# Optimization experiments

Measured on AMD Instinct MI355X. Metric: run time of the kernel, lower is better.

## Reference

```python
import jax, jax.numpy as jnp
import numpy as np

B, S, D = 32, 1, 4096
H, HKV, HD = 32, 8, 128
G = H // HKV            # GQA groups = 4
MAXLEN = 2048
START = 2047            # decode position; cache holds 2047 past tokens


def setup_inputs() -> dict:
    key = jax.random.key(0)
    ks = jax.random.split(key, 8)
    w_scale = 0.02
    # RoPE angles for position START (module works only for seq_len==1)
    inv_freq = 1.0 / (10000.0 ** (np.arange(0, HD, 2, dtype=np.float32) / HD))
    ang = jnp.asarray(START * inv_freq, dtype=jnp.float32)  # (HD/2,)
    return {
        "x": jax.random.normal(ks[0], (B, S, D), jnp.float32),
        "cache_k": jax.random.normal(ks[1], (B, HKV, MAXLEN, HD), jnp.float32),
        "cache_v": jax.random.normal(ks[2], (B, HKV, MAXLEN, HD), jnp.float32),
        "wq": jax.random.normal(ks[3], (D, H * HD), jnp.float32) * w_scale,
        "wk": jax.random.normal(ks[4], (D, HKV * HD), jnp.float32) * w_scale,
        "wv": jax.random.normal(ks[5], (D, HKV * HD), jnp.float32) * w_scale,
        "wo": jax.random.normal(ks[6], (H * HD, D), jnp.float32) * w_scale,
        "freqs_cos": jnp.cos(ang),
        "freqs_sin": jnp.sin(ang),
        "start_pos": START,
    }


def _rope(x, cos, sin):
    # x: (B, h, S, HD); complex multiply on interleaved (even=real, odd=imag) pairs
    xr, xi = x[..., 0::2], x[..., 1::2]
    out_r = xr * cos - xi * sin
    out_i = xr * sin + xi * cos
    return jnp.stack([out_r, out_i], axis=-1).reshape(x.shape)


def reference(x, cache_k, cache_v, wq, wk, wv, wo, freqs_cos, freqs_sin, start_pos):
    b, s, _ = x.shape
    # projections -> (B, heads, S, HD)
    q = (x @ wq).reshape(b, s, H, HD).transpose(0, 2, 1, 3)
    k = (x @ wk).reshape(b, s, HKV, HD).transpose(0, 2, 1, 3)
    v = (x @ wv).reshape(b, s, HKV, HD).transpose(0, 2, 1, 3)
    # RoPE on q and k
    q = _rope(q, freqs_cos, freqs_sin)
    k = _rope(k, freqs_cos, freqs_sin)
    # KV-cache append at start_pos
    ck = jax.lax.dynamic_update_slice(cache_k, k, (0, 0, start_pos, 0))
    cv = jax.lax.dynamic_update_slice(cache_v, v, (0, 0, start_pos, 0))
    L = start_pos + s
    keys = ck[:, :, :L]   # (B, HKV, L, HD)
    vals = cv[:, :, :L]
    # GQA: group query heads over kv heads (avoids materializing repeat_kv;
    # identical math to expand+reshape in the original)
    qg = q.reshape(b, HKV, G, s, HD)
    scale = 1.0 / np.sqrt(HD).astype(np.float32)
    scores = jnp.einsum('bkgsd,bkld->bkgsl', qg, keys) * scale
    probs = jax.nn.softmax(scores.astype(jnp.float32), axis=-1).astype(q.dtype)
    out = jnp.einsum('bkgsl,bkld->bkgsd', probs, vals)
    out = out.reshape(b, H, s, HD).transpose(0, 2, 1, 3).reshape(b, s, H * HD)
    return out @ wo
```

## Files before the change

kernel.cpp:

```cpp
#include <hip/hip_runtime.h>
#include <cmath>

#define Bb 32
#define Dm 4096
#define Hh 32
#define HKVh 8
#define HD 128
#define Gq 4
#define MAXLEN 2048
#define NQ 4096
#define NKV 1024
#define NTOT 6144
#define KSPLIT 8
#define KCH 512
#define LSPLIT 4
#define SCALE 0.08838834764831845f

__device__ __forceinline__ float4 fma4(float s, float4 w, float4 a) {
    a.x = fmaf(s, w.x, a.x); a.y = fmaf(s, w.y, a.y);
    a.z = fmaf(s, w.z, a.z); a.w = fmaf(s, w.w, a.w);
    return a;
}

__global__ __launch_bounds__(256) void k_qkv(const float* __restrict__ x,
    const float* __restrict__ wq, const float* __restrict__ wk,
    const float* __restrict__ wv, float* __restrict__ part)
{
    __shared__ float xs[Bb][KCH];
    const int ct = blockIdx.x;
    const int ks = blockIdx.y;
    const int c0 = ct * 64;
    const int k0 = ks * KCH;
    const float* Wp; int ldw; int cw;
    if (c0 < NQ)          { Wp = wq; ldw = NQ;  cw = c0; }
    else if (c0 < NQ+NKV) { Wp = wk; ldw = NKV; cw = c0 - NQ; }
    else                  { Wp = wv; ldw = NKV; cw = c0 - NQ - NKV; }

    const int t = threadIdx.x;
    for (int i = t; i < Bb * (KCH/4); i += 256) {
        int b = i >> 7;
        int kk = (i & 127) << 2;
        float4 v4 = *(const float4*)(x + (size_t)b*Dm + k0 + kk);
        xs[b][kk+0] = v4.x; xs[b][kk+1] = v4.y; xs[b][kk+2] = v4.z; xs[b][kk+3] = v4.w;
    }
    __syncthreads();

    const int cg = t & 15;
    const int bg = t >> 4;
    const int b0 = bg * 2;
    const float* wp = Wp + (size_t)k0 * ldw + cw + cg*4;
    float4 a0 = make_float4(0.f,0.f,0.f,0.f), a1 = make_float4(0.f,0.f,0.f,0.f);
#pragma unroll 2
    for (int k = 0; k < KCH; k += 4) {
        float4 w0 = *(const float4*)(wp);
        float4 w1 = *(const float4*)(wp + ldw);
        float4 w2 = *(const float4*)(wp + 2*ldw);
        float4 w3 = *(const float4*)(wp + 3*ldw);
        wp += 4*ldw;
        float4 xa = *(const float4*)(&xs[b0][k]);
        float4 xb = *(const float4*)(&xs[b0+1][k]);
        a0 = fma4(xa.x, w0, a0); a1 = fma4(xb.x, w0, a1);
        a0 = fma4(xa.y, w1, a0); a1 = fma4(xb.y, w1, a1);
        a0 = fma4(xa.z, w2, a0); a1 = fma4(xb.z, w2, a1);
        a0 = fma4(xa.w, w3, a0); a1 = fma4(xb.w, w3, a1);
    }
    size_t base = ((size_t)ks * Bb + b0) * NTOT + c0 + cg*4;
    *(float4*)(part + base) = a0;
    *(float4*)(part + base + NTOT) = a1;
}

__global__ __launch_bounds__(256) void k_rope_scatter(const float* __restrict__ part,
    const float* __restrict__ cos_, const float* __restrict__ sin_,
    const int* __restrict__ start_pos, float* __restrict__ qbuf,
    float* __restrict__ cache_k, float* __restrict__ cache_v)
{
    int idx = blockIdx.x*256 + threadIdx.x;
    int b  = idx / (NTOT/2);
    int cp = idx % (NTOT/2);
    int c = cp*2;
    float xr = 0.f, xi = 0.f;
#pragma unroll
    for (int s = 0; s < KSPLIT; ++s) {
        const float2 p = *(const float2*)(part + ((size_t)s*Bb + b)*NTOT + c);
        xr += p.x; xi += p.y;
    }
    const int sp = start_pos[0];
    if (c < NQ) {
        int h = c / HD, dd = c % HD; int fi = dd >> 1;
        float co = cos_[fi], si = sin_[fi];
        float2 o = make_float2(xr*co - xi*si, xr*si + xi*co);
        *(float2*)(qbuf + ((size_t)b*Hh + h)*HD + dd) = o;
    } else if (c < NQ+NKV) {
        int cc = c - NQ; int h = cc / HD, dd = cc % HD; int fi = dd >> 1;
        float co = cos_[fi], si = sin_[fi];
        float2 o = make_float2(xr*co - xi*si, xr*si + xi*co);
        *(float2*)(cache_k + (((size_t)b*HKVh + h)*MAXLEN + sp)*HD + dd) = o;
    } else {
        int cc = c - NQ - NKV; int h = cc / HD, dd = cc % HD;
        *(float2*)(cache_v + (((size_t)b*HKVh + h)*MAXLEN + sp)*HD + dd) = make_float2(xr, xi);
    }
}

__global__ __launch_bounds__(512) void k_attn(const float* __restrict__ qbuf,
    const float* __restrict__ cache_k, const float* __restrict__ cache_v,
    const int* __restrict__ start_pos, float* __restrict__ pout)
{
    __shared__ float sbuf[Gq][128];
    __shared__ float mrun[Gq], lrun[Gq], alphaS[Gq];
    __shared__ float pbuf[4][Gq][HD];

    const int bk = blockIdx.x;
    const int b  = bk >> 3;
    const int kv = bk & 7;
    const int sp = blockIdx.y;
    const int L  = start_pos[0] + 1;
    const int per = (L + LSPLIT - 1) / LSPLIT;
    const int p0 = sp * per;
    const int p1 = min(L, p0 + per);

    const int t = threadIdx.x;
    const int wave = t >> 6;
    const int lane = t & 63;
    const int half = lane >> 5;
    const int dl = lane & 31;

    float4 q4[Gq];
#pragma unroll
    for (int g = 0; g < Gq; ++g)
        q4[g] = *(const float4*)(qbuf + ((size_t)b*Hh + kv*Gq + g)*HD + dl*4);

    const float* kbase = cache_k + ((size_t)b*HKVh + kv)*MAXLEN*HD;
    const float* vbase = cache_v + ((size_t)b*HKVh + kv)*MAXLEN*HD;

    const int dC = t & 127;
    const int psC = t >> 7;
    float acc[Gq] = {0.f,0.f,0.f,0.f};

    if (t < Gq) { mrun[t] = -INFINITY; lrun[t] = 0.f; }
    __syncthreads();

    for (int c0 = p0; c0 < p1; c0 += 128) {
        const int CP = min(128, p1 - c0);
        for (int j = wave; j < 64; j += 8) {
            int p = c0 + 2*j + half;
            int pc = p < p1 ? p : (p1 - 1);
            float4 k4 = *(const float4*)(kbase + (size_t)pc*HD + dl*4);
            float s0 = q4[0].x*k4.x + q4[0].y*k4.y + q4[0].z*k4.z + q4[0].w*k4.w;
            float s1 = q4[1].x*k4.x + q4[1].y*k4.y + q4[1].z*k4.z + q4[1].w*k4.w;
            float s2 = q4[2].x*k4.x + q4[2].y*k4.y + q4[2].z*k4.z + q4[2].w*k4.w;
            float s3 = q4[3].x*k4.x + q4[3].y*k4.y + q4[3].z*k4.z + q4[3].w*k4.w;
#pragma unroll
            for (int off = 16; off; off >>= 1) {
                s0 += __shfl_xor(s0, off, 32);
                s1 += __shfl_xor(s1, off, 32);
                s2 += __shfl_xor(s2, off, 32);
                s3 += __shfl_xor(s3, off, 32);
            }
            if (dl == 0) {
                int slot = 2*j + half;
                bool ok = (p < p1);
                sbuf[0][slot] = ok ? s0*SCALE : -INFINITY;
                sbuf[1][slot] = ok ? s1*SCALE : -INFINITY;
                sbuf[2][slot] = ok ? s2*SCALE : -INFINITY;
                sbuf[3][slot] = ok ? s3*SCALE : -INFINITY;
            }
        }
        __syncthreads();
        if (wave < Gq) {
            int g = wave;
            float s0 = sbuf[g][lane];
            float s1 = sbuf[g][lane + 64];
            float mloc = fmaxf(s0, s1);
#pragma unroll
            for (int off = 32; off; off >>= 1) mloc = fmaxf(mloc, __shfl_xor(mloc, off));
            float mold = mrun[g];
            float mnew = fmaxf(mold, mloc);
            float e0 = __expf(s0 - mnew);
            float e1 = __expf(s1 - mnew);
            sbuf[g][lane]      = e0;
            sbuf[g][lane + 64] = e1;
            float ssum = e0 + e1;
#pragma unroll
            for (int off = 32; off; off >>= 1) ssum += __shfl_xor(ssum, off);
            if (lane == 0) {
                float alpha = (mold == -INFINITY) ? 0.f : __expf(mold - mnew);
                alphaS[g] = alpha;
                lrun[g] = lrun[g]*alpha + ssum;
                mrun[g] = mnew;
            }
        }
        __syncthreads();
        {
#pragma unroll
            for (int g = 0; g < Gq; ++g) acc[g] *= alphaS[g];
            for (int p = c0 + psC; p < c0 + CP; p += 4) {
                float vv = vbase[(size_t)p*HD + dC];
#pragma unroll
                for (int g = 0; g < Gq; ++g)
                    acc[g] = fmaf(sbuf[g][p - c0], vv, acc[g]);
            }
        }
        __syncthreads();
    }
#pragma unroll
    for (int g = 0; g < Gq; ++g) pbuf[psC][g][dC] = acc[g];
    __syncthreads();
    float* po = pout + (size_t)(bk * LSPLIT + sp) * (Gq*HD + 2*Gq);
    {
        int g = t >> 7, d = t & 127;
        float s = pbuf[0][g][d] + pbuf[1][g][d] + pbuf[2][g][d] + pbuf[3][g][d];
        po[g*HD + d] = s;
    }
    if (t < Gq) { po[Gq*HD + t] = mrun[t]; po[Gq*HD + Gq + t] = lrun[t]; }
}

__global__ __launch_bounds__(256) void k_comb(const float* __restrict__ pout,
    float* __restrict__ attn)
{
    int idx = blockIdx.x*256 + threadIdx.x;
    int d = idx & 127;
    int h = (idx >> 7) & 31;
    int b = idx >> 12;
    int kv = h >> 2, g = h & 3;
    int bk = b*8 + kv;
    const float* base = pout + (size_t)bk * LSPLIT * (Gq*HD + 2*Gq);
    float m = -INFINITY;
#pragma unroll
    for (int s = 0; s < LSPLIT; ++s) m = fmaxf(m, base[s*520 + 512 + g]);
    float num = 0.f, den = 0.f;
#pragma unroll
    for (int s = 0; s < LSPLIT; ++s) {
        float ms = base[s*520 + 512 + g];
        float ls = base[s*520 + 516 + g];
        float w = (ms == -INFINITY) ? 0.f : __expf(ms - m);
        num = fmaf(w, base[s*520 + g*HD + d], num);
        den = fmaf(w, ls, den);
    }
    attn[idx] = num / den;
}

__global__ __launch_bounds__(256) void k_proj(const float* __restrict__ inp,
    const float* __restrict__ W, float* __restrict__ part)
{
    __shared__ float xs[Bb][KCH];
    const int ct = blockIdx.x;
    const int ks = blockIdx.y;
    const int c0 = ct * 64;
    const int k0 = ks * KCH;

    const int t = threadIdx.x;
    for (int i = t; i < Bb * (KCH/4); i += 256) {
        int b = i >> 7;
        int kk = (i & 127) << 2;
        float4 v4 = *(const float4*)(inp + (size_t)b*NQ + k0 + kk);
        xs[b][kk+0] = v4.x; xs[b][kk+1] = v4.y; xs[b][kk+2] = v4.z; xs[b][kk+3] = v4.w;
    }
    __syncthreads();

    const int cg = t & 15;
    const int bg = t >> 4;
    const int b0 = bg * 2;
    const float* wp = W + (size_t)k0 * NQ + c0 + cg*4;
    float4 a0 = make_float4(0.f,0.f,0.f,0.f), a1 = make_float4(0.f,0.f,0.f,0.f);
#pragma unroll 2
    for (int k = 0; k < KCH; k += 4) {
        float4 w0 = *(const float4*)(wp);
        float4 w1 = *(const float4*)(wp + NQ);
        float4 w2 = *(const float4*)(wp + 2*NQ);
        float4 w3 = *(const float4*)(wp + 3*NQ);
        wp += 4*NQ;
        float4 xa = *(const float4*)(&xs[b0][k]);
        float4 xb = *(const float4*)(&xs[b0+1][k]);
        a0 = fma4(xa.x, w0, a0); a1 = fma4(xb.x, w0, a1);
        a0 = fma4(xa.y, w1, a0); a1 = fma4(xb.y, w1, a1);
        a0 = fma4(xa.z, w2, a0); a1 = fma4(xb.z, w2, a1);
        a0 = fma4(xa.w, w3, a0); a1 = fma4(xb.w, w3, a1);
    }
    size_t base = ((size_t)ks * Bb + b0) * NQ + c0 + cg*4;
    *(float4*)(part + base) = a0;
    *(float4*)(part + base + NQ) = a1;
}

__global__ __launch_bounds__(256) void k_red(const float* __restrict__ part,
    float* __restrict__ out)
{
    int idx = blockIdx.x*256 + threadIdx.x;
    float s = 0.f;
#pragma unroll
    for (int k = 0; k < KSPLIT; ++k) s += part[(size_t)k*Bb*NQ + idx];
    out[idx] = s;
}

extern "C" void kernel_launch(void* const* d_in, const int* in_sizes, int n_in,
                              void* d_out, int out_size, void* d_ws, size_t ws_size,
                              hipStream_t stream)
{
    const float* x  = (const float*)d_in[0];
    float* cache_k  = (float*)d_in[1];
    float* cache_v  = (float*)d_in[2];
    const float* wq = (const float*)d_in[3];
    const float* wk = (const float*)d_in[4];
    const float* wv = (const float*)d_in[5];
    const float* wo = (const float*)d_in[6];
    const float* fc = (const float*)d_in[7];
    const float* fs = (const float*)d_in[8];
    const int* sp   = (const int*)d_in[9];
    float* out      = (float*)d_out;

    float* ws = (float*)d_ws;
    float* qkv_part = ws;
    float* qbuf     = qkv_part + 1572864;
    float* attn_prt = qbuf + 131072;
    float* attn_out = attn_prt + 532480;
    float* proj_prt = attn_out + 131072;

    k_qkv<<<dim3(96, 8), 256, 0, stream>>>(x, wq, wk, wv, qkv_part);
    k_rope_scatter<<<dim3(384), 256, 0, stream>>>(qkv_part, fc, fs, sp, qbuf, cache_k, cache_v);
    k_attn<<<dim3(256, LSPLIT), 512, 0, stream>>>(qbuf, cache_k, cache_v, sp, attn_prt);
    k_comb<<<dim3(512), 256, 0, stream>>>(attn_prt, attn_out);
    k_proj<<<dim3(64, 8), 256, 0, stream>>>(attn_out, wo, proj_prt);
    k_red<<<dim3(512), 256, 0, stream>>>(proj_prt, out);
}
```

Measured before the change: 751.6 us.

## Restructure decode attention into per-wave online softmax without block barriers

Each of the 8 waves in the attention block now owns a contiguous slice of the sequence range. Within that slice it streams K and V together, keeps the running max, sum and output accumulator in registers, and folds the softmax scale into q. This replaces the earlier per-128-position chunk loop, which staged scores in shared memory behind three block-wide barriers and used a separate pass for the softmax and the V accumulation. Partial results are merged once, first across the two half-waves and then across waves through shared memory. The aim is to remove barrier stalls and overlap K and V memory traffic. The cost is more exp calls per position and higher register pressure from float4 accumulators for four groups.

```diff
diff --git a/kernel.cpp b/kernel.cpp
--- a/kernel.cpp
+++ b/kernel.cpp
@@ -105,9 +105,9 @@
     const float* __restrict__ cache_k, const float* __restrict__ cache_v,
     const int* __restrict__ start_pos, float* __restrict__ pout)
 {
-    __shared__ float sbuf[Gq][128];
-    __shared__ float mrun[Gq], lrun[Gq], alphaS[Gq];
-    __shared__ float pbuf[4][Gq][HD];
+    __shared__ float sm[8][Gq];
+    __shared__ float sl[8][Gq];
+    __shared__ float sacc[8][Gq][HD];
 
     const int bk = blockIdx.x;
     const int b  = bk >> 3;
@@ -122,96 +122,130 @@
     const int wave = t >> 6;
     const int lane = t & 63;
     const int half = lane >> 5;
-    const int dl = lane & 31;
+    const int dl   = lane & 31;
 
     float4 q4[Gq];
 #pragma unroll
-    for (int g = 0; g < Gq; ++g)
-        q4[g] = *(const float4*)(qbuf + ((size_t)b*Hh + kv*Gq + g)*HD + dl*4);
+    for (int g = 0; g < Gq; ++g) {
+        float4 qq = *(const float4*)(qbuf + ((size_t)b*Hh + kv*Gq + g)*HD + dl*4);
+        qq.x *= SCALE; qq.y *= SCALE; qq.z *= SCALE; qq.w *= SCALE;
+        q4[g] = qq;
+    }
 
     const float* kbase = cache_k + ((size_t)b*HKVh + kv)*MAXLEN*HD;
     const float* vbase = cache_v + ((size_t)b*HKVh + kv)*MAXLEN*HD;
 
-    const int dC = t & 127;
-    const int psC = t >> 7;
-    float acc[Gq] = {0.f,0.f,0.f,0.f};
-
-    if (t < Gq) { mrun[t] = -INFINITY; lrun[t] = 0.f; }
+    const int nw  = (per + 7) >> 3;
+    const int wp0 = p0 + wave * nw;
+    const int wp1 = min(p1, wp0 + nw);
+
+    float  m[Gq], l[Gq];
+    float4 acc[Gq];
+#pragma unroll
+    for (int g = 0; g < Gq; ++g) {
+        m[g] = -1e30f; l[g] = 0.f;
+        acc[g] = make_float4(0.f, 0.f, 0.f, 0.f);
+    }
+
+    for (int pp = wp0; pp < wp1; pp += 4) {
+        const int pa = pp + half;
+        const int pb = pp + 2 + half;
+        const bool va = pa < wp1;
+        const bool vb = pb < wp1;
+        const int pca = va ? pa : wp0;
+        const int pcb = vb ? pb : wp0;
+        const float4 kA = *(const float4*)(kbase + (size_t)pca*HD + dl*4);
+        const float4 kB = *(const float4*)(kbase + (size_t)pcb*HD + dl*4);
+        const float4 vA = *(const float4*)(vbase + (size_t)pca*HD + dl*4);
+        const float4 vB = *(const float4*)(vbase + (size_t)pcb*HD + dl*4);
+
+        float sA[Gq], sB[Gq];
+#pragma unroll
+        for (int g = 0; g < Gq; ++g) {
+            sA[g] = q4[g].x*kA.x + q4[g].y*kA.y + q4[g].z*kA.z + q4[g].w*kA.w;
+            sB[g] = q4[g].x*kB.x + q4[g].y*kB.y + q4[g].z*kB.z + q4[g].w*kB.w;
+        }
+#pragma unroll
+        for (int off = 16; off; off >>= 1) {
+#pragma unroll
+            for (int g = 0; g < Gq; ++g) {
+                sA[g] += __shfl_xor(sA[g], off);
+                sB[g] += __shfl_xor(sB[g], off);
+            }
+        }
+        if (!va) { sA[0] = -INFINITY; sA[1] = -INFINITY; sA[2] = -INFINITY; sA[3] = -INFINITY; }
+        if (!vb) { sB[0] = -INFINITY; sB[1] = -INFINITY; sB[2] = -INFINITY; sB[3] = -INFINITY; }
+
+#pragma unroll
+        for (int g = 0; g < Gq; ++g) {
+            float mn = fmaxf(m[g], sA[g]);
+            float al = __expf(m[g] - mn);
+            float e  = __expf(sA[g] - mn);
+            m[g] = mn;
+            l[g] = l[g]*al + e;
+            acc[g].x = fmaf(e, vA.x, acc[g].x*al);
+            acc[g].y = fmaf(e, vA.y, acc[g].y*al);
+            acc[g].z = fmaf(e, vA.z, acc[g].z*al);
+            acc[g].w = fmaf(e, vA.w, acc[g].w*al);
+        }
+#pragma unroll
+        for (int g = 0; g < Gq; ++g) {
+            float mn = fmaxf(m[g], sB[g]);
+            float al = __expf(m[g] - mn);
+            float e  = __expf(sB[g] - mn);
+            m[g] = mn;
+            l[g] = l[g]*al + e;
+            acc[g].x = fmaf(e, vB.x, acc[g].x*al);
+            acc[g].y = fmaf(e, vB.y, acc[g].y*al);
+            acc[g].z = fmaf(e, vB.z, acc[g].z*al);
+            acc[g].w = fmaf(e, vB.w, acc[g].w*al);
+        }
+    }
+
+#pragma unroll
+    for (int g = 0; g < Gq; ++g) {
+        float mo = __shfl_xor(m[g], 32);
+        float lo = __shfl_xor(l[g], 32);
+        float ax = __shfl_xor(acc[g].x, 32);
+        float ay = __shfl_xor(acc[g].y, 32);
+        float az = __shfl_xor(acc[g].z, 32);
+        float aw = __shfl_xor(acc[g].w, 32);
+        float mn = fmaxf(m[g], mo);
+        float a0 = __expf(m[g] - mn);
+        float a1 = __expf(mo - mn);
+        m[g] = mn;
+        l[g] = l[g]*a0 + lo*a1;
+        acc[g].x = acc[g].x*a0 + ax*a1;
+        acc[g].y = acc[g].y*a0 + ay*a1;
+        acc[g].z = acc[g].z*a0 + az*a1;
+        acc[g].w = acc[g].w*a0 + aw*a1;
+    }
+
+    if (half == 0) {
+#pragma unroll
+        for (int g = 0; g < Gq; ++g) {
+            *(float4*)(&sacc[wave][g][dl*4]) = acc[g];
+            if (dl == 0) { sm[wave][g] = m[g]; sl[wave][g] = l[g]; }
+        }
+    }
     __syncthreads();
 
-    for (int c0 = p0; c0 < p1; c0 += 128) {
-        const int CP = min(128, p1 - c0);
-        for (int j = wave; j < 64; j += 8) {
-            int p = c0 + 2*j + half;
-            int pc = p < p1 ? p : (p1 - 1);
-            float4 k4 = *(const float4*)(kbase + (size_t)pc*HD + dl*4);
-            float s0 = q4[0].x*k4.x + q4[0].y*k4.y + q4[0].z*k4.z + q4[0].w*k4.w;
-            float s1 = q4[1].x*k4.x + q4[1].y*k4.y + q4[1].z*k4.z + q4[1].w*k4.w;
-            float s2 = q4[2].x*k4.x + q4[2].y*k4.y + q4[2].z*k4.z + q4[2].w*k4.w;
-            float s3 = q4[3].x*k4.x + q4[3].y*k4.y + q4[3].z*k4.z + q4[3].w*k4.w;
-#pragma unroll
-            for (int off = 16; off; off >>= 1) {
-                s0 += __shfl_xor(s0, off, 32);
-                s1 += __shfl_xor(s1, off, 32);
-                s2 += __shfl_xor(s2, off, 32);
-                s3 += __shfl_xor(s3, off, 32);
-            }
-            if (dl == 0) {
-                int slot = 2*j + half;
-                bool ok = (p < p1);
-                sbuf[0][slot] = ok ? s0*SCALE : -INFINITY;
-                sbuf[1][slot] = ok ? s1*SCALE : -INFINITY;
-                sbuf[2][slot] = ok ? s2*SCALE : -INFINITY;
-                sbuf[3][slot] = ok ? s3*SCALE : -INFINITY;
-            }
-        }
-        __syncthreads();
-        if (wave < Gq) {
-            int g = wave;
-            float s0 = sbuf[g][lane];
-            float s1 = sbuf[g][lane + 64];
-            float mloc = fmaxf(s0, s1);
-#pragma unroll
-            for (int off = 32; off; off >>= 1) mloc = fmaxf(mloc, __shfl_xor(mloc, off));
-            float mold = mrun[g];
-            float mnew = fmaxf(mold, mloc);
-            float e0 = __expf(s0 - mnew);
-            float e1 = __expf(s1 - mnew);
-            sbuf[g][lane]      = e0;
-            sbuf[g][lane + 64] = e1;
-            float ssum = e0 + e1;
-#pragma unroll
-            for (int off = 32; off; off >>= 1) ssum += __shfl_xor(ssum, off);
-            if (lane == 0) {
-                float alpha = (mold == -INFINITY) ? 0.f : __expf(mold - mnew);
-                alphaS[g] = alpha;
-                lrun[g] = lrun[g]*alpha + ssum;
-                mrun[g] = mnew;
-            }
-        }
-        __syncthreads();
-        {
-#pragma unroll
-            for (int g = 0; g < Gq; ++g) acc[g] *= alphaS[g];
-            for (int p = c0 + psC; p < c0 + CP; p += 4) {
-                float vv = vbase[(size_t)p*HD + dC];
-#pragma unroll
-                for (int g = 0; g < Gq; ++g)
-                    acc[g] = fmaf(sbuf[g][p - c0], vv, acc[g]);
-            }
-        }
-        __syncthreads();
-    }
-#pragma unroll
-    for (int g = 0; g < Gq; ++g) pbuf[psC][g][dC] = acc[g];
-    __syncthreads();
-    float* po = pout + (size_t)(bk * LSPLIT + sp) * (Gq*HD + 2*Gq);
     {
-        int g = t >> 7, d = t & 127;
-        float s = pbuf[0][g][d] + pbuf[1][g][d] + pbuf[2][g][d] + pbuf[3][g][d];
-        po[g*HD + d] = s;
-    }
-    if (t < Gq) { po[Gq*HD + t] = mrun[t]; po[Gq*HD + Gq + t] = lrun[t]; }
+        const int g = t >> 7, d = t & 127;
+        float M = -1e30f;
+#pragma unroll
+        for (int w = 0; w < 8; ++w) M = fmaxf(M, sm[w][g]);
+        float num = 0.f, den = 0.f;
+#pragma unroll
+        for (int w = 0; w < 8; ++w) {
+            float wt = __expf(sm[w][g] - M);
+            num = fmaf(wt, sacc[w][g][d], num);
+            den = fmaf(wt, sl[w][g], den);
+        }
+        float* po = pout + (size_t)(bk * LSPLIT + sp) * (Gq*HD + 2*Gq);
+        po[g*HD + d] = num;
+        if (d == 0) { po[Gq*HD + g] = M; po[Gq*HD + Gq + g] = den; }
+    }
 }
 
 __global__ __launch_bounds__(256) void k_comb(const float* __restrict__ pout,
```

Result: faster. 726.6 us (-3.3%).
